# Optimization experiments

Measured on AMD Instinct MI355X. Metric: run time of the kernel, lower is better.

The kernel has to match this reference:

```python
import jax, jax.numpy as jnp
import numpy as np

ALPHA = 0.5
SMOOTH = 1e-05
ITERS = 10


def _max_pool3x3(x):
    # 3x3 max pool, stride 1, SAME padding on NCHW tensor
    return jax.lax.reduce_window(
        x, -jnp.inf, jax.lax.max,
        window_dimensions=(1, 1, 3, 3),
        window_strides=(1, 1, 1, 1),
        padding='SAME')


def _soft_erode(x):
    return -_max_pool3x3(-x)


def _soft_dilate(x):
    return _max_pool3x3(x)


def _soft_skeletonize(img, iterations=ITERS):
    def body(skel, _):
        eroded = _soft_erode(skel)
        temp = _soft_dilate(eroded)
        skel = skel - (skel - eroded) * temp
        skel = jnp.clip(skel, 0.0, 1.0)
        return skel, None
    skel, _ = jax.lax.scan(body, img, None, length=iterations)
    return skel


def _dice_score(pred, target, smooth=SMOOTH):
    inter = jnp.sum(pred * target, axis=(2, 3))
    union = jnp.sum(pred, axis=(2, 3)) + jnp.sum(target, axis=(2, 3))
    dice = (2.0 * inter + smooth) / (union + smooth)
    return jnp.mean(dice)


def setup_inputs() -> dict:
    key = jax.random.key(0)
    k1, k2 = jax.random.split(key)
    B, C, H, W = 32, 1, 512, 512
    pred_logits = jax.random.normal(k1, (B, C, H, W), dtype=jnp.float32)
    target = jax.random.uniform(k2, (B, C, H, W), dtype=jnp.float32)
    return {"pred_logits": pred_logits, "target": target}


def reference(pred_logits, target):
    pred = jax.nn.sigmoid(pred_logits)
    dice = _dice_score(pred, target)
    pred_skel = _soft_skeletonize(pred)
    target_skel = _soft_skeletonize(target)
    skel_dice = _dice_score(pred_skel, target_skel)
    loss = (1.0 - ALPHA) * (1.0 - dice) + ALPHA * (1.0 - skel_dice)
    return (loss, dice, skel_dice)
```

## Files before the change

kernel.cpp:

```cpp
#include <hip/hip_runtime.h>
#include <hip/hip_fp16.h>
#include <math.h>


#define H 512
#define W 512
#define IMG (H * W)
#define NIMG 64
#define NPRED 32

#define APITCH 80
#define AROWS 74
#define BP2 38
#define BROWS 68

typedef _Float16 f16;
typedef __fp16 fp16v2 __attribute__((ext_vector_type(2)));

__device__ __forceinline__ float2 unpack2(uint u) {
    fp16v2 h = __builtin_bit_cast(fp16v2, u);
    return make_float2((float)h.x, (float)h.y);
}
__device__ __forceinline__ uint pack2(float a, float b) {
    fp16v2 h = __builtin_amdgcn_cvt_pkrtz(a, b);
    return __builtin_bit_cast(uint, h);
}

__device__ __forceinline__ float wsum64(float v) {
#pragma unroll
    for (int o = 32; o > 0; o >>= 1) v += __shfl_down(v, o);
    return v;
}

__device__ __forceinline__ void hmin3(const float* __restrict__ row, float h[6],
                                      float4& q1out) {
    float4 q0 = *(const float4*)(row);
    float4 q1 = *(const float4*)(row + 4);
    float4 q2 = *(const float4*)(row + 8);
    q1out = q1;
    h[0] = fminf(q0.z, fminf(q0.w, q1.x));
    h[1] = fminf(q0.w, fminf(q1.x, q1.y));
    h[2] = fminf(q1.x, fminf(q1.y, q1.z));
    h[3] = fminf(q1.y, fminf(q1.z, q1.w));
    h[4] = fminf(q1.z, fminf(q1.w, q2.x));
    h[5] = fminf(q1.w, fminf(q2.x, q2.y));
}

__device__ __forceinline__ void hmin3h(const uint* __restrict__ row, float h[6],
                                       float4& q1out) {
    uint2 a = *(const uint2*)(row);
    uint2 b = *(const uint2*)(row + 2);
    uint2 d = *(const uint2*)(row + 4);
    float2 p1 = unpack2(a.y);
    float2 p2 = unpack2(b.x);
    float2 p3 = unpack2(b.y);
    float2 p4 = unpack2(d.x);
    q1out = make_float4(p2.x, p2.y, p3.x, p3.y);
    h[0] = fminf(p1.x, fminf(p1.y, p2.x));
    h[1] = fminf(p1.y, fminf(p2.x, p2.y));
    h[2] = fminf(p2.x, fminf(p2.y, p3.x));
    h[3] = fminf(p2.y, fminf(p3.x, p3.y));
    h[4] = fminf(p3.x, fminf(p3.y, p4.x));
    h[5] = fminf(p3.y, fminf(p4.x, p4.y));
}

__device__ __forceinline__ void erode1(const float a[6], const float b[6], const float c[6],
                                       bool rowok, const bool cm[6], float e[6]) {
#pragma unroll
    for (int j = 0; j < 6; j++) {
        float v = fminf(a[j], fminf(b[j], c[j]));
        e[j] = (rowok && cm[j]) ? v : -INFINITY;
    }
}

__device__ __forceinline__ void erode2(const float a[6], const float b[6], const float c[6],
                                       int gy, bool lo, bool ro, float e[6]) {
    bool oob = (gy < 0) || (gy >= H);
#pragma unroll
    for (int j = 0; j < 6; j++) {
        float v = fminf(a[j], fminf(b[j], c[j]));
        e[j] = oob ? -INFINITY : v;
    }
    if (lo) e[0] = -INFINITY;
    if (ro) e[5] = -INFINITY;
}

__device__ __forceinline__ void hmax1(const float e[6], float hx[4], float ec[4]) {
    hx[0] = fmaxf(e[0], fmaxf(e[1], e[2]));
    hx[1] = fmaxf(e[1], fmaxf(e[2], e[3]));
    hx[2] = fmaxf(e[2], fmaxf(e[3], e[4]));
    hx[3] = fmaxf(e[3], fmaxf(e[4], e[5]));
    ec[0] = e[1]; ec[1] = e[2]; ec[2] = e[3]; ec[3] = e[4];
}

template<int SIG>
__device__ void fillA_f32(float* __restrict__ A, const float* __restrict__ src,
                          int tileX, int tileY, int tid) {
    const float PINF = INFINITY;
    for (int it = tid; it < AROWS * 20; it += 256) {
        int r = it / 20;
        int c = it - r * 20;
        int gy = tileY + r - 4;
        int gx = tileX + 4 * c - 8;
        float4 v = make_float4(PINF, PINF, PINF, PINF);
        if ((unsigned)(c - 1) < 18u && (unsigned)gy < (unsigned)H &&
            (unsigned)gx < (unsigned)W) {
            v = *(const float4*)(src + (size_t)gy * W + gx);
            if (SIG) {
                v.x = 1.0f / (1.0f + __expf(-v.x));
                v.y = 1.0f / (1.0f + __expf(-v.y));
                v.z = 1.0f / (1.0f + __expf(-v.z));
                v.w = 1.0f / (1.0f + __expf(-v.w));
            }
        }
        *(float4*)(A + r * APITCH + 4 * c) = v;
    }
}

__device__ void fillA_f16(float* __restrict__ A, const f16* __restrict__ src,
                          int tileX, int tileY, int tid) {
    const float PINF = INFINITY;
    for (int it = tid; it < AROWS * 20; it += 256) {
        int r = it / 20;
        int c = it - r * 20;
        int gy = tileY + r - 4;
        int gx = tileX + 4 * c - 8;
        float4 v = make_float4(PINF, PINF, PINF, PINF);
        if ((unsigned)(c - 1) < 18u && (unsigned)gy < (unsigned)H &&
            (unsigned)gx < (unsigned)W) {
            uint2 g = *(const uint2*)(src + (size_t)gy * W + gx);
            float2 lo = unpack2(g.x), hi = unpack2(g.y);
            v = make_float4(lo.x, lo.y, hi.x, hi.y);
        }
        *(float4*)(A + r * APITCH + 4 * c) = v;
    }
}

__device__ void stage1(const float* __restrict__ A, uint* __restrict__ Bu,
                       int tileX, int tileY, int tid) {
    for (int item = tid; item < 252; item += 256) {
        const int s = item / 18;
        const int q = item - s * 18;
        const int gcb = tileX - 4 + 4 * q;
        const int ys = tileY - 2 + 5 * s;
        bool cm[6], sm[4];
#pragma unroll
        for (int j = 0; j < 6; j++) cm[j] = ((unsigned)(gcb - 1 + j) < (unsigned)W);
#pragma unroll
        for (int j = 0; j < 4; j++) sm[j] = ((unsigned)(gcb + j) < (unsigned)W);
        const int lr = 5 * s + 2;
        const float* Ab = A + 4 * q;
        float hm[3][6], hx[3][4], e[6], ec_cur[4], ec_nxt[4];
        float4 scq[3], qd;
        hmin3(Ab + (lr - 2) * APITCH, hm[0], qd);
        hmin3(Ab + (lr - 1) * APITCH, hm[1], qd);
        hmin3(Ab + (lr + 0) * APITCH, hm[2], scq[0]);
        erode1(hm[0], hm[1], hm[2], (unsigned)(ys - 1) < (unsigned)H, cm, e);
        hmax1(e, hx[0], ec_nxt);
        hmin3(Ab + (lr + 1) * APITCH, hm[0], scq[1]);
        erode1(hm[1], hm[2], hm[0], (unsigned)ys < (unsigned)H, cm, e);
        hmax1(e, hx[1], ec_cur);
#pragma unroll
        for (int k = 0; k < 5; k++) {
            hmin3(Ab + (lr + 2 + k) * APITCH, hm[(k + 1) % 3], scq[(2 + k) % 3]);
            erode1(hm[(k + 2) % 3], hm[k % 3], hm[(k + 1) % 3],
                   (unsigned)(ys + k + 1) < (unsigned)H, cm, e);
            hmax1(e, hx[(k + 2) % 3], ec_nxt);
            float t0 = fmaxf(hx[k % 3][0], fmaxf(hx[(k + 1) % 3][0], hx[(k + 2) % 3][0]));
            float t1 = fmaxf(hx[k % 3][1], fmaxf(hx[(k + 1) % 3][1], hx[(k + 2) % 3][1]));
            float t2 = fmaxf(hx[k % 3][2], fmaxf(hx[(k + 1) % 3][2], hx[(k + 2) % 3][2]));
            float t3 = fmaxf(hx[k % 3][3], fmaxf(hx[(k + 1) % 3][3], hx[(k + 2) % 3][3]));
            float4 sc = scq[k % 3];
            float o0 = fminf(fmaxf(sc.x - (sc.x - ec_cur[0]) * t0, 0.0f), 1.0f);
            float o1 = fminf(fmaxf(sc.y - (sc.y - ec_cur[1]) * t1, 0.0f), 1.0f);
            float o2 = fminf(fmaxf(sc.z - (sc.z - ec_cur[2]) * t2, 0.0f), 1.0f);
            float o3 = fminf(fmaxf(sc.w - (sc.w - ec_cur[3]) * t3, 0.0f), 1.0f);
            int br = 5 * s + k;
            if (br < BROWS) {
                bool rin = ((unsigned)(ys + k) < (unsigned)H);
                float v0 = (rin && sm[0]) ? o0 : INFINITY;
                float v1 = (rin && sm[1]) ? o1 : INFINITY;
                float v2 = (rin && sm[2]) ? o2 : INFINITY;
                float v3 = (rin && sm[3]) ? o3 : INFINITY;
                uint2 wv;
                wv.x = pack2(v0, v1);
                wv.y = pack2(v2, v3);
                *(uint2*)(Bu + br * BP2 + 2 * q) = wv;
            }
            ec_cur[0] = ec_nxt[0]; ec_cur[1] = ec_nxt[1];
            ec_cur[2] = ec_nxt[2]; ec_cur[3] = ec_nxt[3];
        }
    }
}

template<bool TOREG>
__device__ void stage2(const uint* __restrict__ Bu, int tileX, int tileY,
                       int tx, int ty, f16* __restrict__ gdst, float (*oreg)[4]) {
    const int X = tileX + 4 * tx;
    const int gy0 = tileY + 4 * ty;
    const int rb = 4 * ty + 2;
    const bool lo = (X == 0);
    const bool ro = (X + 4 >= W);
    const uint* Bb = Bu + 2 * tx;
    float hm[3][6], hx[3][4], e[6], ec_cur[4], ec_nxt[4];
    float4 scq[3], qd;
    hmin3h(Bb + (rb - 2) * BP2, hm[0], qd);
    hmin3h(Bb + (rb - 1) * BP2, hm[1], qd);
    hmin3h(Bb + (rb + 0) * BP2, hm[2], scq[0]);
    erode2(hm[0], hm[1], hm[2], gy0 - 1, lo, ro, e);
    hmax1(e, hx[0], ec_nxt);
    hmin3h(Bb + (rb + 1) * BP2, hm[0], scq[1]);
    erode2(hm[1], hm[2], hm[0], gy0, lo, ro, e);
    hmax1(e, hx[1], ec_cur);
#pragma unroll
    for (int k = 0; k < 4; k++) {
        hmin3h(Bb + (rb + 2 + k) * BP2, hm[(k + 1) % 3], scq[(2 + k) % 3]);
        erode2(hm[(k + 2) % 3], hm[k % 3], hm[(k + 1) % 3], gy0 + k + 1, lo, ro, e);
        hmax1(e, hx[(k + 2) % 3], ec_nxt);
        float t0 = fmaxf(hx[k % 3][0], fmaxf(hx[(k + 1) % 3][0], hx[(k + 2) % 3][0]));
        float t1 = fmaxf(hx[k % 3][1], fmaxf(hx[(k + 1) % 3][1], hx[(k + 2) % 3][1]));
        float t2 = fmaxf(hx[k % 3][2], fmaxf(hx[(k + 1) % 3][2], hx[(k + 2) % 3][2]));
        float t3 = fmaxf(hx[k % 3][3], fmaxf(hx[(k + 1) % 3][3], hx[(k + 2) % 3][3]));
        float4 sc = scq[k % 3];
        float4 o;
        o.x = fminf(fmaxf(sc.x - (sc.x - ec_cur[0]) * t0, 0.0f), 1.0f);
        o.y = fminf(fmaxf(sc.y - (sc.y - ec_cur[1]) * t1, 0.0f), 1.0f);
        o.z = fminf(fmaxf(sc.z - (sc.z - ec_cur[2]) * t2, 0.0f), 1.0f);
        o.w = fminf(fmaxf(sc.w - (sc.w - ec_cur[3]) * t3, 0.0f), 1.0f);
        if (TOREG) {
            oreg[k][0] = o.x; oreg[k][1] = o.y; oreg[k][2] = o.z; oreg[k][3] = o.w;
        } else {
            uint2 w;
            w.x = pack2(o.x, o.y);
            w.y = pack2(o.z, o.w);
            *(uint2*)(gdst + (size_t)(gy0 + k) * W + X) = w;
        }
        ec_cur[0] = ec_nxt[0]; ec_cur[1] = ec_nxt[1];
        ec_cur[2] = ec_nxt[2]; ec_cur[3] = ec_nxt[3];
    }
}

__global__ __launch_bounds__(256, 4) void k_first(
    const float* __restrict__ logits, const float* __restrict__ target,
    f16* __restrict__ outb, float* __restrict__ parts0, float* __restrict__ parts1) {
    __shared__ float A[AROWS * APITCH];
    __shared__ uint Bu[BROWS * BP2];
    __shared__ float red[8];
    const int img = blockIdx.z;
    const int tileX = blockIdx.x * 64, tileY = blockIdx.y * 64;
    const int tid = threadIdx.y * 16 + threadIdx.x;
    const bool pred = (img < NPRED);
    if (pred) fillA_f32<1>(A, logits + (size_t)img * IMG, tileX, tileY, tid);
    else      fillA_f32<0>(A, target + (size_t)(img - NPRED) * IMG, tileX, tileY, tid);
    __syncthreads();
    float a = 0.0f, b = 0.0f;
    if (pred) {
        const float* tgt = target + (size_t)img * IMG;
        for (int i = tid; i < 1024; i += 256) {
            int r = i >> 4, c4 = (i & 15) * 4;
            float4 p = *(const float4*)(A + (r + 4) * APITCH + c4 + 8);
            float4 t = *(const float4*)(tgt + (size_t)(tileY + r) * W + tileX + c4);
            a += p.x * t.x + p.y * t.y + p.z * t.z + p.w * t.w;
            b += p.x + p.y + p.z + p.w;
        }
    } else {
        for (int i = tid; i < 1024; i += 256) {
            int r = i >> 4, c4 = (i & 15) * 4;
            float4 t = *(const float4*)(A + (r + 4) * APITCH + c4 + 8);
            a += t.x + t.y + t.z + t.w;
        }
    }
    a = wsum64(a); b = wsum64(b);
    if ((tid & 63) == 0) { red[tid >> 6] = a; red[4 + (tid >> 6)] = b; }
    stage1(A, Bu, tileX, tileY, tid);
    __syncthreads();
    if (tid == 0) {
        int bi = blockIdx.z * 64 + blockIdx.y * 8 + blockIdx.x;
        parts0[bi] = red[0] + red[1] + red[2] + red[3];
        parts1[bi] = red[4] + red[5] + red[6] + red[7];
    }
    stage2<false>(Bu, tileX, tileY, threadIdx.x, threadIdx.y,
                  outb + (size_t)img * IMG, nullptr);
}

__global__ __launch_bounds__(256, 4) void k_mid(
    const f16* __restrict__ in, f16* __restrict__ outb) {
    __shared__ float A[AROWS * APITCH];
    __shared__ uint Bu[BROWS * BP2];
    const int img = blockIdx.z;
    const int tileX = blockIdx.x * 64, tileY = blockIdx.y * 64;
    const int tid = threadIdx.y * 16 + threadIdx.x;
    fillA_f16(A, in + (size_t)img * IMG, tileX, tileY, tid);
    __syncthreads();
    stage1(A, Bu, tileX, tileY, tid);
    __syncthreads();
    stage2<false>(Bu, tileX, tileY, threadIdx.x, threadIdx.y,
                  outb + (size_t)img * IMG, nullptr);
}

__global__ __launch_bounds__(256, 4) void k_last(
    const f16* __restrict__ in, float* __restrict__ pA,
    float* __restrict__ pB, float* __restrict__ pC) {
    __shared__ float A[AROWS * APITCH];
    __shared__ uint Bu[BROWS * BP2];
    __shared__ float red[12];
    const int img = blockIdx.z;
    const int tileX = blockIdx.x * 64, tileY = blockIdx.y * 64;
    const int tid = threadIdx.y * 16 + threadIdx.x;
    float op[4][4], ot[4][4];
    fillA_f16(A, in + (size_t)img * IMG, tileX, tileY, tid);
    __syncthreads();
    stage1(A, Bu, tileX, tileY, tid);
    __syncthreads();
    stage2<true>(Bu, tileX, tileY, threadIdx.x, threadIdx.y, nullptr, op);
    fillA_f16(A, in + (size_t)(img + NPRED) * IMG, tileX, tileY, tid);
    __syncthreads();
    stage1(A, Bu, tileX, tileY, tid);
    __syncthreads();
    stage2<true>(Bu, tileX, tileY, threadIdx.x, threadIdx.y, nullptr, ot);
    float a = 0.0f, b = 0.0f, c = 0.0f;
#pragma unroll
    for (int k = 0; k < 4; k++)
#pragma unroll
        for (int j = 0; j < 4; j++) {
            a += op[k][j] * ot[k][j];
            b += op[k][j];
            c += ot[k][j];
        }
    a = wsum64(a); b = wsum64(b); c = wsum64(c);
    if ((tid & 63) == 0) {
        red[tid >> 6] = a; red[4 + (tid >> 6)] = b; red[8 + (tid >> 6)] = c;
    }
    __syncthreads();
    if (tid == 0) {
        int bi = img * 64 + blockIdx.y * 8 + blockIdx.x;
        pA[bi] = red[0] + red[1] + red[2] + red[3];
        pB[bi] = red[4] + red[5] + red[6] + red[7];
        pC[bi] = red[8] + red[9] + red[10] + red[11];
    }
}

__global__ __launch_bounds__(64) void finalize_img(
    const float* __restrict__ parts0, const float* __restrict__ parts1,
    const float* __restrict__ pA, const float* __restrict__ pB,
    const float* __restrict__ pC, float* __restrict__ dices) {
    const int i = blockIdx.x, t = threadIdx.x;
    float inter = wsum64(parts0[i * 64 + t]);
    float sp = wsum64(parts1[i * 64 + t]);
    float st = wsum64(parts0[(NPRED + i) * 64 + t]);
    float i2 = wsum64(pA[i * 64 + t]);
    float sp2 = wsum64(pB[i * 64 + t]);
    float st2 = wsum64(pC[i * 64 + t]);
    if (t == 0) {
        dices[i] = (float)((2.0 * (double)inter + 1e-5) / ((double)sp + (double)st + 1e-5));
        dices[32 + i] = (float)((2.0 * (double)i2 + 1e-5) / ((double)sp2 + (double)st2 + 1e-5));
    }
}

__global__ void finalize_out(const float* __restrict__ dices, float* __restrict__ out) {
    const int t = threadIdx.x;
    double d = 0.0, sd = 0.0;
    if (t < 32) { d = dices[t]; sd = dices[32 + t]; }
#pragma unroll
    for (int o = 32; o > 0; o >>= 1) { d += __shfl_down(d, o); sd += __shfl_down(sd, o); }
    if (t == 0) {
        d *= (1.0 / 32.0); sd *= (1.0 / 32.0);
        out[0] = (float)(0.5 * (1.0 - d) + 0.5 * (1.0 - sd));
        out[1] = (float)d;
        out[2] = (float)sd;
    }
}

extern "C" void kernel_launch(void* const* d_in, const int* in_sizes, int n_in,
                              void* d_out, int out_size, void* d_ws, size_t ws_size,
                              hipStream_t stream) {
    (void)in_sizes; (void)n_in; (void)out_size; (void)ws_size;
    const float* logits = (const float*)d_in[0];
    const float* target = (const float*)d_in[1];
    float* out = (float*)d_out;
    f16* buf0 = (f16*)d_ws;
    f16* buf1 = buf0 + (size_t)NIMG * IMG;
    float* parts0 = (float*)(buf1 + (size_t)NIMG * IMG);
    float* parts1 = parts0 + 4096;
    float* pA = parts1 + 4096;
    float* pB = pA + 2048;
    float* pC = pB + 2048;
    float* dices = pC + 2048;

    dim3 blk(16, 16, 1);
    k_first<<<dim3(8, 8, NIMG), blk, 0, stream>>>(logits, target, buf0, parts0, parts1);
    k_mid<<<dim3(8, 8, NIMG), blk, 0, stream>>>(buf0, buf1);
    k_mid<<<dim3(8, 8, NIMG), blk, 0, stream>>>(buf1, buf0);
    k_mid<<<dim3(8, 8, NIMG), blk, 0, stream>>>(buf0, buf1);
    k_last<<<dim3(8, 8, NPRED), blk, 0, stream>>>(buf1, pA, pB, pC);
    finalize_img<<<32, 64, 0, stream>>>(parts0, parts1, pA, pB, pC, dices);
    finalize_out<<<1, 64, 0, stream>>>(dices, out);
}
```

Measured before the change: 261.9 us.

## Store shared input tile as packed fp16 and fuse dice sums into fill

The shared A tile now holds packed fp16 pairs instead of fp32, roughly halving its LDS footprint. The mid kernels copy fp16 global data straight into LDS with no unpack and repack, and stage1 reads it through the half-precision hmin3 path. The first kernel now accumulates the dice partial sums during the fill loop instead of a separate pass, and launch bounds rise from 4 to 7 blocks per CU to use the freed LDS. The first iteration's input is now rounded to fp16 before the first erosion, a small accuracy change, and the higher occupancy target may squeeze registers.

```diff
diff --git a/kernel.cpp b/kernel.cpp
--- a/kernel.cpp
+++ b/kernel.cpp
@@ -1,5 +1,4 @@
 #include <hip/hip_runtime.h>
-#include <hip/hip_fp16.h>
 #include <math.h>
 
 
@@ -9,11 +8,13 @@
 #define NIMG 64
 #define NPRED 32
 
-#define APITCH 80
+#define AP 42
 #define AROWS 74
 #define BP2 38
 #define BROWS 68
 
+#define PINF_U 0x7C007C00u
+
 typedef _Float16 f16;
 typedef __fp16 fp16v2 __attribute__((ext_vector_type(2)));
 
@@ -30,20 +31,6 @@
 #pragma unroll
     for (int o = 32; o > 0; o >>= 1) v += __shfl_down(v, o);
     return v;
-}
-
-__device__ __forceinline__ void hmin3(const float* __restrict__ row, float h[6],
-                                      float4& q1out) {
-    float4 q0 = *(const float4*)(row);
-    float4 q1 = *(const float4*)(row + 4);
-    float4 q2 = *(const float4*)(row + 8);
-    q1out = q1;
-    h[0] = fminf(q0.z, fminf(q0.w, q1.x));
-    h[1] = fminf(q0.w, fminf(q1.x, q1.y));
-    h[2] = fminf(q1.x, fminf(q1.y, q1.z));
-    h[3] = fminf(q1.y, fminf(q1.z, q1.w));
-    h[4] = fminf(q1.z, fminf(q1.w, q2.x));
-    h[5] = fminf(q1.w, fminf(q2.x, q2.y));
 }
 
 __device__ __forceinline__ void hmin3h(const uint* __restrict__ row, float h[6],
@@ -93,50 +80,55 @@
     ec[0] = e[1]; ec[1] = e[2]; ec[2] = e[3]; ec[3] = e[4];
 }
 
-template<int SIG>
-__device__ void fillA_f32(float* __restrict__ A, const float* __restrict__ src,
-                          int tileX, int tileY, int tid) {
-    const float PINF = INFINITY;
+template<int PRED>
+__device__ void fill_f32(uint* __restrict__ A, const float* __restrict__ src,
+                         const float* __restrict__ tgt, int tileX, int tileY, int tid,
+                         float& da, float& db) {
     for (int it = tid; it < AROWS * 20; it += 256) {
-        int r = it / 20;
-        int c = it - r * 20;
+        int r = it / 20, c = it - r * 20;
         int gy = tileY + r - 4;
         int gx = tileX + 4 * c - 8;
-        float4 v = make_float4(PINF, PINF, PINF, PINF);
+        uint2 v = make_uint2(PINF_U, PINF_U);
         if ((unsigned)(c - 1) < 18u && (unsigned)gy < (unsigned)H &&
             (unsigned)gx < (unsigned)W) {
-            v = *(const float4*)(src + (size_t)gy * W + gx);
-            if (SIG) {
-                v.x = 1.0f / (1.0f + __expf(-v.x));
-                v.y = 1.0f / (1.0f + __expf(-v.y));
-                v.z = 1.0f / (1.0f + __expf(-v.z));
-                v.w = 1.0f / (1.0f + __expf(-v.w));
+            float4 f = *(const float4*)(src + (size_t)gy * W + gx);
+            if (PRED) {
+                f.x = 1.0f / (1.0f + __expf(-f.x));
+                f.y = 1.0f / (1.0f + __expf(-f.y));
+                f.z = 1.0f / (1.0f + __expf(-f.z));
+                f.w = 1.0f / (1.0f + __expf(-f.w));
+            }
+            v.x = pack2(f.x, f.y);
+            v.y = pack2(f.z, f.w);
+            if ((unsigned)(r - 4) < 64u && (unsigned)(c - 2) < 16u) {
+                if (PRED) {
+                    float4 t = *(const float4*)(tgt + (size_t)gy * W + gx);
+                    da += f.x * t.x + f.y * t.y + f.z * t.z + f.w * t.w;
+                    db += f.x + f.y + f.z + f.w;
+                } else {
+                    da += f.x + f.y + f.z + f.w;
+                }
             }
         }
-        *(float4*)(A + r * APITCH + 4 * c) = v;
-    }
-}
-
-__device__ void fillA_f16(float* __restrict__ A, const f16* __restrict__ src,
-                          int tileX, int tileY, int tid) {
-    const float PINF = INFINITY;
+        *(uint2*)(A + r * AP + 2 * c) = v;
+    }
+}
+
+__device__ void fill_h(uint* __restrict__ A, const uint* __restrict__ src,
+                       int tileX, int tileY, int tid) {
     for (int it = tid; it < AROWS * 20; it += 256) {
-        int r = it / 20;
-        int c = it - r * 20;
+        int r = it / 20, c = it - r * 20;
         int gy = tileY + r - 4;
         int gx = tileX + 4 * c - 8;
-        float4 v = make_float4(PINF, PINF, PINF, PINF);
+        uint2 v = make_uint2(PINF_U, PINF_U);
         if ((unsigned)(c - 1) < 18u && (unsigned)gy < (unsigned)H &&
-            (unsigned)gx < (unsigned)W) {
-            uint2 g = *(const uint2*)(src + (size_t)gy * W + gx);
-            float2 lo = unpack2(g.x), hi = unpack2(g.y);
-            v = make_float4(lo.x, lo.y, hi.x, hi.y);
-        }
-        *(float4*)(A + r * APITCH + 4 * c) = v;
-    }
-}
-
-__device__ void stage1(const float* __restrict__ A, uint* __restrict__ Bu,
+            (unsigned)gx < (unsigned)W)
+            v = *(const uint2*)(src + gy * (W / 2) + (gx >> 1));
+        *(uint2*)(A + r * AP + 2 * c) = v;
+    }
+}
+
+__device__ void stage1(const uint* __restrict__ A, uint* __restrict__ Bu,
                        int tileX, int tileY, int tid) {
     for (int item = tid; item < 252; item += 256) {
         const int s = item / 18;
@@ -149,20 +141,20 @@
 #pragma unroll
         for (int j = 0; j < 4; j++) sm[j] = ((unsigned)(gcb + j) < (unsigned)W);
         const int lr = 5 * s + 2;
-        const float* Ab = A + 4 * q;
+        const uint* Ab = A + 2 * q;
         float hm[3][6], hx[3][4], e[6], ec_cur[4], ec_nxt[4];
         float4 scq[3], qd;
-        hmin3(Ab + (lr - 2) * APITCH, hm[0], qd);
-        hmin3(Ab + (lr - 1) * APITCH, hm[1], qd);
-        hmin3(Ab + (lr + 0) * APITCH, hm[2], scq[0]);
+        hmin3h(Ab + (lr - 2) * AP, hm[0], qd);
+        hmin3h(Ab + (lr - 1) * AP, hm[1], qd);
+        hmin3h(Ab + (lr + 0) * AP, hm[2], scq[0]);
         erode1(hm[0], hm[1], hm[2], (unsigned)(ys - 1) < (unsigned)H, cm, e);
         hmax1(e, hx[0], ec_nxt);
-        hmin3(Ab + (lr + 1) * APITCH, hm[0], scq[1]);
+        hmin3h(Ab + (lr + 1) * AP, hm[0], scq[1]);
         erode1(hm[1], hm[2], hm[0], (unsigned)ys < (unsigned)H, cm, e);
         hmax1(e, hx[1], ec_cur);
 #pragma unroll
         for (int k = 0; k < 5; k++) {
-            hmin3(Ab + (lr + 2 + k) * APITCH, hm[(k + 1) % 3], scq[(2 + k) % 3]);
+            hmin3h(Ab + (lr + 2 + k) * AP, hm[(k + 1) % 3], scq[(2 + k) % 3]);
             erode1(hm[(k + 2) % 3], hm[k % 3], hm[(k + 1) % 3],
                    (unsigned)(ys + k + 1) < (unsigned)H, cm, e);
             hmax1(e, hx[(k + 2) % 3], ec_nxt);
@@ -195,7 +187,7 @@
 
 template<bool TOREG>
 __device__ void stage2(const uint* __restrict__ Bu, int tileX, int tileY,
-                       int tx, int ty, f16* __restrict__ gdst, float (*oreg)[4]) {
+                       int tx, int ty, uint* __restrict__ gdst, float (*oreg)[4]) {
     const int X = tileX + 4 * tx;
     const int gy0 = tileY + 4 * ty;
     const int rb = 4 * ty + 2;
@@ -233,91 +225,78 @@
             uint2 w;
             w.x = pack2(o.x, o.y);
             w.y = pack2(o.z, o.w);
-            *(uint2*)(gdst + (size_t)(gy0 + k) * W + X) = w;
+            *(uint2*)(gdst + (size_t)(gy0 + k) * (W / 2) + (X >> 1)) = w;
         }
         ec_cur[0] = ec_nxt[0]; ec_cur[1] = ec_nxt[1];
         ec_cur[2] = ec_nxt[2]; ec_cur[3] = ec_nxt[3];
     }
 }
 
-__global__ __launch_bounds__(256, 4) void k_first(
+__global__ __launch_bounds__(256, 7) void k_first(
     const float* __restrict__ logits, const float* __restrict__ target,
-    f16* __restrict__ outb, float* __restrict__ parts0, float* __restrict__ parts1) {
-    __shared__ float A[AROWS * APITCH];
-    __shared__ uint Bu[BROWS * BP2];
+    uint* __restrict__ outb, float* __restrict__ parts0, float* __restrict__ parts1) {
+    __shared__ uint A[AROWS * AP];
+    __shared__ uint B[BROWS * BP2];
     __shared__ float red[8];
     const int img = blockIdx.z;
     const int tileX = blockIdx.x * 64, tileY = blockIdx.y * 64;
     const int tid = threadIdx.y * 16 + threadIdx.x;
-    const bool pred = (img < NPRED);
-    if (pred) fillA_f32<1>(A, logits + (size_t)img * IMG, tileX, tileY, tid);
-    else      fillA_f32<0>(A, target + (size_t)(img - NPRED) * IMG, tileX, tileY, tid);
-    __syncthreads();
     float a = 0.0f, b = 0.0f;
-    if (pred) {
-        const float* tgt = target + (size_t)img * IMG;
-        for (int i = tid; i < 1024; i += 256) {
-            int r = i >> 4, c4 = (i & 15) * 4;
-            float4 p = *(const float4*)(A + (r + 4) * APITCH + c4 + 8);
-            float4 t = *(const float4*)(tgt + (size_t)(tileY + r) * W + tileX + c4);
-            a += p.x * t.x + p.y * t.y + p.z * t.z + p.w * t.w;
-            b += p.x + p.y + p.z + p.w;
-        }
-    } else {
-        for (int i = tid; i < 1024; i += 256) {
-            int r = i >> 4, c4 = (i & 15) * 4;
-            float4 t = *(const float4*)(A + (r + 4) * APITCH + c4 + 8);
-            a += t.x + t.y + t.z + t.w;
-        }
-    }
+    if (img < NPRED)
+        fill_f32<1>(A, logits + (size_t)img * IMG, target + (size_t)img * IMG,
+                    tileX, tileY, tid, a, b);
+    else
+        fill_f32<0>(A, target + (size_t)(img - NPRED) * IMG, nullptr,
+                    tileX, tileY, tid, a, b);
     a = wsum64(a); b = wsum64(b);
     if ((tid & 63) == 0) { red[tid >> 6] = a; red[4 + (tid >> 6)] = b; }
-    stage1(A, Bu, tileX, tileY, tid);
+    __syncthreads();
+    stage1(A, B, tileX, tileY, tid);
     __syncthreads();
     if (tid == 0) {
         int bi = blockIdx.z * 64 + blockIdx.y * 8 + blockIdx.x;
         parts0[bi] = red[0] + red[1] + red[2] + red[3];
         parts1[bi] = red[4] + red[5] + red[6] + red[7];
     }
-    stage2<false>(Bu, tileX, tileY, threadIdx.x, threadIdx.y,
-                  outb + (size_t)img * IMG, nullptr);
-}
-
-__global__ __launch_bounds__(256, 4) void k_mid(
-    const f16* __restrict__ in, f16* __restrict__ outb) {
-    __shared__ float A[AROWS * APITCH];
-    __shared__ uint Bu[BROWS * BP2];
+    stage2<false>(B, tileX, tileY, threadIdx.x, threadIdx.y,
+                  outb + (size_t)img * (IMG / 2), nullptr);
+}
+
+__global__ __launch_bounds__(256, 7) void k_mid(
+    const uint* __restrict__ in, uint* __restrict__ outb) {
+    __shared__ uint A[AROWS * AP];
+    __shared__ uint B[BROWS * BP2];
     const int img = blockIdx.z;
     const int tileX = blockIdx.x * 64, tileY = blockIdx.y * 64;
     const int tid = threadIdx.y * 16 + threadIdx.x;
-    fillA_f16(A, in + (size_t)img * IMG, tileX, tileY, tid);
-    __syncthreads();
-    stage1(A, Bu, tileX, tileY, tid);
-    __syncthreads();
-    stage2<false>(Bu, tileX, tileY, threadIdx.x, threadIdx.y,
-                  outb + (size_t)img * IMG, nullptr);
-}
-
-__global__ __launch_bounds__(256, 4) void k_last(
-    const f16* __restrict__ in, float* __restrict__ pA,
+    fill_h(A, in + (size_t)img * (IMG / 2), tileX, tileY, tid);
+    __syncthreads();
+    stage1(A, B, tileX, tileY, tid);
+    __syncthreads();
+    stage2<false>(B, tileX, tileY, threadIdx.x, threadIdx.y,
+                  outb + (size_t)img * (IMG / 2), nullptr);
+}
+
+__global__ __launch_bounds__(256, 7) void k_last(
+    const uint* __restrict__ in, float* __restrict__ pA,
     float* __restrict__ pB, float* __restrict__ pC) {
-    __shared__ float A[AROWS * APITCH];
-    __shared__ uint Bu[BROWS * BP2];
+    __shared__ uint A[AROWS * AP];
+    __shared__ uint B[BROWS * BP2];
     __shared__ float red[12];
     const int img = blockIdx.z;
     const int tileX = blockIdx.x * 64, tileY = blockIdx.y * 64;
     const int tid = threadIdx.y * 16 + threadIdx.x;
     float op[4][4], ot[4][4];
-    fillA_f16(A, in + (size_t)img * IMG, tileX, tileY, tid);
-    __syncthreads();
-    stage1(A, Bu, tileX, tileY, tid);
-    __syncthreads();
-    stage2<true>(Bu, tileX, tileY, threadIdx.x, threadIdx.y, nullptr, op);
-    fillA_f16(A, in + (size_t)(img + NPRED) * IMG, tileX, tileY, tid);
-    __syncthreads();
-    stage1(A, Bu, tileX, tileY, tid);
-    __syncthreads();
-    stage2<true>(Bu, tileX, tileY, threadIdx.x, threadIdx.y, nullptr, ot);
+    fill_h(A, in + (size_t)img * (IMG / 2), tileX, tileY, tid);
+    __syncthreads();
+    stage1(A, B, tileX, tileY, tid);
+    __syncthreads();
+    stage2<true>(B, tileX, tileY, threadIdx.x, threadIdx.y, nullptr, op);
+    fill_h(A, in + (size_t)(img + NPRED) * (IMG / 2), tileX, tileY, tid);
+    __syncthreads();
+    stage1(A, B, tileX, tileY, tid);
+    __syncthreads();
+    stage2<true>(B, tileX, tileY, threadIdx.x, threadIdx.y, nullptr, ot);
     float a = 0.0f, b = 0.0f, c = 0.0f;
 #pragma unroll
     for (int k = 0; k < 4; k++)
@@ -378,9 +357,9 @@
     const float* logits = (const float*)d_in[0];
     const float* target = (const float*)d_in[1];
     float* out = (float*)d_out;
-    f16* buf0 = (f16*)d_ws;
-    f16* buf1 = buf0 + (size_t)NIMG * IMG;
-    float* parts0 = (float*)(buf1 + (size_t)NIMG * IMG);
+    uint* buf0 = (uint*)d_ws;
+    uint* buf1 = buf0 + (size_t)NIMG * (IMG / 2);
+    float* parts0 = (float*)(buf1 + (size_t)NIMG * (IMG / 2));
     float* parts1 = parts0 + 4096;
     float* pA = parts1 + 4096;
     float* pB = pA + 2048;
```

Result: slower. 291.1 us (+11.2%).
